# Performance work log

Measured on AMD Instinct MI355X. Metric: run time of the kernel, lower is better.

The kernel has to match this reference:

```python
import jax, jax.numpy as jnp
import numpy as np

N = 20000      # nodes
E = 320000     # edges (avg degree 16)
F_IN = 14
F_OUT = 9
H = 128        # hidden
L = 6          # message passing layers
ED = 3         # edge_dim
MSG_IN = 2 * H + ED  # 259


def _w(k, shape):
    return jax.random.normal(k, shape, jnp.float32) / np.sqrt(shape[0]).astype(np.float32)


def setup_inputs() -> dict:
    key = jax.random.key(0)
    ks = jax.random.split(key, 16)
    x = jax.random.normal(ks[0], (N, F_IN), jnp.float32)
    edge_index = jax.random.randint(ks[1], (2, E), 0, N, jnp.int64)
    edge_attr = jax.random.normal(ks[2], (E, ED), jnp.float32)
    # encoder: Linear(14,128) -> SiLU -> Linear(128,128)
    enc_w1 = _w(ks[3], (F_IN, H)); enc_b1 = jnp.zeros((H,), jnp.float32)
    enc_w2 = _w(ks[4], (H, H));    enc_b2 = jnp.zeros((H,), jnp.float32)
    # L EdgeConv layers: MLP(259->128) -> SiLU -> (128->128), stacked on leading dim
    kc = jax.random.split(ks[5], 2 * L)
    conv_w1 = jnp.stack([_w(kc[i], (MSG_IN, H)) for i in range(L)])
    conv_b1 = jnp.zeros((L, H), jnp.float32)
    conv_w2 = jnp.stack([_w(kc[L + i], (H, H)) for i in range(L)])
    conv_b2 = jnp.zeros((L, H), jnp.float32)
    # decoder: 128->128 SiLU 128->64 SiLU 64->9
    dec_w1 = _w(ks[6], (H, H));       dec_b1 = jnp.zeros((H,), jnp.float32)
    dec_w2 = _w(ks[7], (H, H // 2));  dec_b2 = jnp.zeros((H // 2,), jnp.float32)
    dec_w3 = _w(ks[8], (H // 2, F_OUT)); dec_b3 = jnp.zeros((F_OUT,), jnp.float32)
    return dict(x=x, edge_index=edge_index, edge_attr=edge_attr,
                enc_w1=enc_w1, enc_b1=enc_b1, enc_w2=enc_w2, enc_b2=enc_b2,
                conv_w1=conv_w1, conv_b1=conv_b1, conv_w2=conv_w2, conv_b2=conv_b2,
                dec_w1=dec_w1, dec_b1=dec_b1, dec_w2=dec_w2, dec_b2=dec_b2,
                dec_w3=dec_w3, dec_b3=dec_b3)


def _mlp2(x, w1, b1, w2, b2):
    return jnp.dot(jax.nn.silu(jnp.dot(x, w1) + b1), w2) + b2


def reference(x, edge_index, edge_attr,
              enc_w1, enc_b1, enc_w2, enc_b2,
              conv_w1, conv_b1, conv_w2, conv_b2,
              dec_w1, dec_b1, dec_w2, dec_b2, dec_w3, dec_b3):
    src, dst = edge_index[0], edge_index[1]
    # in-degree for mean aggregation (computed once; structure is fixed)
    deg = jnp.maximum(
        jax.ops.segment_sum(jnp.ones((E,), jnp.float32), dst, num_segments=N), 1.0)
    h = _mlp2(x, enc_w1, enc_b1, enc_w2, enc_b2)  # (N, H)
    for l in range(L):
        # gather-compute-scatter EdgeConv: msg MLP on [h_dst, h_src, edge_attr]
        m_in = jnp.concatenate([h[dst], h[src], edge_attr], axis=-1)  # (E, 2H+ED)
        m = _mlp2(m_in, conv_w1[l], conv_b1[l], conv_w2[l], conv_b2[l])  # (E, H)
        agg = jax.ops.segment_sum(m, dst, num_segments=N) / deg[:, None]  # (N, H)
        h = h + agg  # residual; dropout is identity in eval mode
    h = jax.nn.silu(jnp.dot(h, dec_w1) + dec_b1)
    h = jax.nn.silu(jnp.dot(h, dec_w2) + dec_b2)
    return jnp.dot(h, dec_w3) + dec_b3  # (N, F_OUT)
```

## Files before the change

### kernel.cpp

```cpp
#include <hip/hip_runtime.h>
#include <hip/hip_bf16.h>

#define NN 20000
#define EE 320000
#define HD 128

typedef _Float16 half8 __attribute__((ext_vector_type(8)));
typedef _Float16 half4 __attribute__((ext_vector_type(4)));
typedef _Float16 half2v __attribute__((ext_vector_type(2)));
typedef float floatx4 __attribute__((ext_vector_type(4)));
typedef float float2v __attribute__((ext_vector_type(2)));

__device__ __forceinline__ float silu_f(float x){
  float e = __expf(-x);
  return x * __builtin_amdgcn_rcpf(1.f + e);
}

__device__ __forceinline__ bool ei_is64(const int* __restrict__ ei){
  return (ei[1] | ei[3] | ei[5] | ei[7]) == 0;
}
__device__ __forceinline__ int ei_src(const int* __restrict__ ei, int e, bool is64){
  return is64 ? ei[2*(size_t)e] : ei[e];
}
__device__ __forceinline__ int ei_dst(const int* __restrict__ ei, int e, bool is64){
  return is64 ? ei[2*(size_t)EE + 2*(size_t)e] : ei[EE + e];
}

__global__ __launch_bounds__(256) void sentinel_kernel(float* __restrict__ out, int n, float val){
  int i = blockIdx.x*256 + threadIdx.x;
  if (i < n) out[i] = val;
}

__global__ __launch_bounds__(256) void pack_all_kernel(const float* __restrict__ cw1,
                                                       const float* __restrict__ cw2,
                                                       const float* __restrict__ dw1,
                                                       const float* __restrict__ dw2,
                                                       _Float16* __restrict__ w1p,
                                                       _Float16* __restrict__ w2p,
                                                       _Float16* __restrict__ w1dp,
                                                       _Float16* __restrict__ w2dp,
                                                       int* __restrict__ cur){
  int idx = blockIdx.x*256 + threadIdx.x;
  if (idx >= 319488){
    int j = idx - 319488;
    if (j < NN) cur[j] = 0;
    return;
  }
  if (idx < 196608){
    int j   = idx & 7;
    int ln  = (idx >> 3) & 63;
    int rest= idx >> 9;
    int cb  = rest & 15;
    int rest2 = rest >> 4;
    int ks  = rest2 & 3;
    int l   = rest2 >> 2;
    int k = ks*32 + (ln>>4)*8 + j;
    int c = cb*16 + (ln&15);
    float v = (c < 128) ? cw1[(size_t)l*33152 + (size_t)k*128 + c]
                        : cw1[(size_t)l*33152 + (size_t)(128+k)*128 + (c-128)];
    w1p[idx] = (_Float16)v;
  } else if (idx < 294912){
    int t = idx - 196608;
    int j   = t & 7;
    int ln  = (t >> 3) & 63;
    int rest= t >> 9;
    int cb  = rest & 7;
    int rest2 = rest >> 3;
    int ks  = rest2 & 3;
    int l   = rest2 >> 2;
    int k = ks*32 + (ln>>4)*8 + j;
    int c = cb*16 + (ln&15);
    w2p[t] = (_Float16)cw2[(size_t)l*16384 + (size_t)k*128 + c];
  } else {
    int t2 = idx - 294912;
    if (t2 < 16384){
      int j = t2 & 7, ln = (t2>>3)&63, cb = (t2>>9)&7, ks = t2>>12;
      int k = ks*32 + (ln>>4)*8 + j;
      int c = cb*16 + (ln&15);
      w1dp[t2] = (_Float16)dw1[(size_t)k*128 + c];
    } else {
      int t = t2 - 16384;
      int j = t & 7, ln = (t>>3)&63, cb = (t>>9)&3, ks = t>>11;
      int k = ks*32 + (ln>>4)*8 + j;
      int c = cb*16 + (ln&15);
      w2dp[t] = (_Float16)dw2[(size_t)k*64 + c];
    }
  }
}

__global__ __launch_bounds__(256) void count_kernel(const int* __restrict__ ei,
                                                    int* __restrict__ cnt,
                                                    int* __restrict__ rank){
  int e = blockIdx.x*256 + threadIdx.x;
  bool is64 = ei_is64(ei);
  rank[e] = atomicAdd(&cnt[ei_dst(ei, e, is64)], 1);
}

__global__ __launch_bounds__(1024) void scan_kernel(const int* __restrict__ cntcur,
                                                    int* __restrict__ row_start,
                                                    float* __restrict__ invd){
  __shared__ int part[1024];
  const int t = threadIdx.x;
  const int base = t*20;
  int loc[20];
  int sum = 0;
  #pragma unroll
  for (int i=0;i<20;++i){
    int n = base+i;
    int v = (n < NN) ? cntcur[n] : 0;
    loc[i] = sum; sum += v;
  }
  part[t] = sum;
  __syncthreads();
  for (int off=1; off<1024; off<<=1){
    int v = (t >= off) ? part[t-off] : 0;
    __syncthreads();
    part[t] += v;
    __syncthreads();
  }
  int pre = (t > 0) ? part[t-1] : 0;
  #pragma unroll
  for (int i=0;i<20;++i){
    int n = base+i;
    if (n < NN){
      int rs = pre + loc[i];
      int deg = ((i<19)?loc[i+1]:sum) - loc[i];
      row_start[n] = rs;
      invd[n] = (deg > 0) ? 1.f/(float)deg : 0.f;
    }
  }
  if (t == 1023) row_start[NN] = part[1023];
}

__global__ __launch_bounds__(128) void scatter_encoder_kernel(
    const int* __restrict__ ei, const float* __restrict__ eattr,
    const int* __restrict__ rstart, const int* __restrict__ rank,
    int4* __restrict__ rec,
    const float* __restrict__ x, const float* __restrict__ w1, const float* __restrict__ b1,
    const float* __restrict__ w2, const float* __restrict__ b2,
    float* __restrict__ h, _Float16* __restrict__ hh)
{
  __shared__ float xs[16][14];
  __shared__ float s1[16][128];
  const int tid = threadIdx.x;

  if (blockIdx.x < 2500){
    int e = blockIdx.x*128 + tid;
    bool is64 = ei_is64(ei);
    int s = ei_src(ei, e, is64);
    int d = ei_dst(ei, e, is64);
    int pos = rstart[d] + rank[e];
    int4 r;
    r.x = __float_as_int(eattr[(size_t)e*3+0]);
    r.y = __float_as_int(eattr[(size_t)e*3+1]);
    r.z = __float_as_int(eattr[(size_t)e*3+2]);
    r.w = s*256;
    rec[pos] = r;
    return;
  }

  const int n0 = (blockIdx.x - 2500)*16;
  for (int idx=tid; idx<224; idx+=128){
    int i = idx/14, k = idx%14;
    xs[i][k] = x[(size_t)(n0+i)*14 + k];
  }
  __syncthreads();
  const int o = tid;
  float acc[16];
  float bv = b1[o];
  #pragma unroll
  for (int i=0;i<16;++i) acc[i] = bv;
  for (int k=0;k<14;++k){
    float w = w1[k*128+o];
    #pragma unroll
    for (int i=0;i<16;++i) acc[i] += xs[i][k]*w;
  }
  #pragma unroll
  for (int i=0;i<16;++i) s1[i][o] = silu_f(acc[i]);
  __syncthreads();
  float bv2 = b2[o];
  #pragma unroll
  for (int i=0;i<16;++i) acc[i] = bv2;
  for (int k=0;k<128;k+=4){
    float w0=w2[(k+0)*128+o], w1v=w2[(k+1)*128+o], w2v=w2[(k+2)*128+o], w3v=w2[(k+3)*128+o];
    #pragma unroll
    for (int i=0;i<16;++i){
      float4 sv = *(const float4*)&s1[i][k];
      acc[i] += sv.x*w0 + sv.y*w1v + sv.z*w2v + sv.w*w3v;
    }
  }
  #pragma unroll
  for (int i=0;i<16;++i){
    size_t off = (size_t)(n0+i)*HD + o;
    h[off] = acc[i];
    hh[off] = (_Float16)acc[i];
  }
}

__global__ __launch_bounds__(256) void proj_kernel(
    const _Float16* __restrict__ hh, const _Float16* __restrict__ w1p,
    const float* __restrict__ b1, _Float16* __restrict__ UV)
{
  const int tid = threadIdx.x;
  const int wv  = tid >> 6;
  const int ln  = tid & 63;
  const int q   = ln >> 4;
  const int m   = ln & 15;
  const int n0  = blockIdx.x*16;

  floatx4 acc[4];
  #pragma unroll
  for (int j=0;j<4;++j) acc[j] = (floatx4){0.f,0.f,0.f,0.f};

  #pragma unroll
  for (int ks=0; ks<4; ++ks){
    half8 a = *(const half8*)(hh + (size_t)(n0+m)*HD + ks*32 + q*8);
    const _Float16* wb = w1p + (size_t)(ks*16*64 + ln)*8;
    #pragma unroll
    for (int j=0; j<4; ++j){
      half8 b = *(const half8*)(wb + (size_t)(wv*4+j)*512);
      acc[j] = __builtin_amdgcn_mfma_f32_16x16x32_f16(a, b, acc[j], 0,0,0);
    }
  }
  #pragma unroll
  for (int j=0; j<4; ++j){
    const int c = (wv*4+j)*16 + m;
    const float bias = (c < 128) ? b1[c] : 0.f;
    #pragma unroll
    for (int r=0;r<4;++r)
      UV[(size_t)(n0+q*4+r)*256 + c] = (_Float16)(acc[j][r] + bias);
  }
}

__device__ __forceinline__ float2v edge_contrib(int4 r, half2v v, float2v u,
                                                float2v wc0, float2v wc1, float2v wc2){
  float2v p = u;
  p += __int_as_float(r.x) * wc0;
  p += __int_as_float(r.y) * wc1;
  p += __int_as_float(r.z) * wc2;
  p[0] += (float)v[0];
  p[1] += (float)v[1];
  float2v s;
  s[0] = silu_f(p[0]);
  s[1] = silu_f(p[1]);
  return s;
}

__global__ __launch_bounds__(1024, 8) void layer_kernel(
    const _Float16* __restrict__ UVc, _Float16* __restrict__ UVn,
    const int* __restrict__ row_start, const int4* __restrict__ rec,
    const float* __restrict__ w1e, const float* __restrict__ invd,
    const _Float16* __restrict__ w2p, const float* __restrict__ b2,
    float* __restrict__ h,
    const _Float16* __restrict__ w1pn, const float* __restrict__ b1n,
    int do_proj,
    const _Float16* __restrict__ w1dp, const float* __restrict__ db1,
    const _Float16* __restrict__ w2dp, const float* __restrict__ db2,
    const float* __restrict__ dw3, const float* __restrict__ db3,
    float* __restrict__ out, int do_dec)
{
  __shared__ _Float16 Sl[16][136];
  __shared__ _Float16 hl[16][136];
  __shared__ __align__(16) char ubuf[8576];
  float    (*dl)[132]  = (float(*)[132])ubuf;
  _Float16 (*d1)[136]  = (_Float16(*)[136])ubuf;
  float    (*s2m)[66]  = (float(*)[66])(ubuf + 4352);

  const int tid = threadIdx.x;
  const int w   = __builtin_amdgcn_readfirstlane(tid >> 6);
  const int ln  = tid & 63;
  const int q   = ln >> 4;
  const int m   = ln & 15;
  const int n0  = blockIdx.x*16;

  {
    const int n  = n0 + w;
    const int c0 = ln*2;
    const float2v wc0 = *(const float2v*)(w1e +   0 + c0);
    const float2v wc1 = *(const float2v*)(w1e + 128 + c0);
    const float2v wc2 = *(const float2v*)(w1e + 256 + c0);

    half2v uvp = *(const half2v*)(UVc + (size_t)n*256 + c0);
    float2v u; u[0] = (float)uvp[0]; u[1] = (float)uvp[1];

    const int rs = row_start[n], re = row_start[n+1];
    float2v a0 = {0.f,0.f}, a1 = {0.f,0.f}, a2 = {0.f,0.f}, a3 = {0.f,0.f};

    const int nq = (re - rs) >> 2;
    int e = rs;
    for (int qq = 0; qq < nq; ++qq, e += 4){
      const int4 r0 = rec[e+0];
      const int4 r1 = rec[e+1];
      const int4 r2 = rec[e+2];
      const int4 r3 = rec[e+3];
      const half2v v0 = *(const half2v*)(UVc + (size_t)r0.w + 128 + c0);
      const half2v v1 = *(const half2v*)(UVc + (size_t)r1.w + 128 + c0);
      const half2v v2 = *(const half2v*)(UVc + (size_t)r2.w + 128 + c0);
      const half2v v3 = *(const half2v*)(UVc + (size_t)r3.w + 128 + c0);
      a0 += edge_contrib(r0, v0, u, wc0, wc1, wc2);
      a1 += edge_contrib(r1, v1, u, wc0, wc1, wc2);
      a2 += edge_contrib(r2, v2, u, wc0, wc1, wc2);
      a3 += edge_contrib(r3, v3, u, wc0, wc1, wc2);
    }
    if (e < re){
      const int e1 = (e+1 < re) ? e+1 : e;
      const int e2 = (e+2 < re) ? e+2 : e;
      const int4 r0 = rec[e];
      const int4 r1 = rec[e1];
      const int4 r2 = rec[e2];
      const half2v v0 = *(const half2v*)(UVc + (size_t)r0.w + 128 + c0);
      const half2v v1 = *(const half2v*)(UVc + (size_t)r1.w + 128 + c0);
      const half2v v2 = *(const half2v*)(UVc + (size_t)r2.w + 128 + c0);
      a0 += edge_contrib(r0, v0, u, wc0, wc1, wc2);
      if (e+1 < re) a1 += edge_contrib(r1, v1, u, wc0, wc1, wc2);
      if (e+2 < re) a2 += edge_contrib(r2, v2, u, wc0, wc1, wc2);
    }
    float2v a = (a0 + a1) + (a2 + a3);
    const float iv = invd[n];
    half2v outv; outv[0] = (_Float16)(a[0]*iv); outv[1] = (_Float16)(a[1]*iv);
    *(half2v*)&Sl[w][c0] = outv;
  }
  __syncthreads();

  if (w < 8){
    floatx4 acc = (floatx4){0.f,0.f,0.f,0.f};
    #pragma unroll
    for (int ks=0; ks<4; ++ks){
      half8 a = *(const half8*)&Sl[m][ks*32 + q*8];
      half8 b = *(const half8*)(w2p + (size_t)(ks*8*64 + ln)*8 + (size_t)w*512);
      acc = __builtin_amdgcn_mfma_f32_16x16x32_f16(a, b, acc, 0,0,0);
    }
    const int c = w*16 + m;
    #pragma unroll
    for (int r=0;r<4;++r) dl[q*4+r][c] = acc[r];
  }
  __syncthreads();

  {
    const int row = w;
    const int col = ln*2;
    const float g = (invd[n0 + row] > 0.f) ? 1.f : 0.f;
    float2 hv = *(const float2*)&h[(size_t)(n0+row)*HD + col];
    float2 bv = *(const float2*)&b2[col];
    float2 dv = *(const float2*)&dl[row][col];
    hv.x += dv.x + g*bv.x;
    hv.y += dv.y + g*bv.y;
    if (!do_dec)
      *(float2*)&h[(size_t)(n0+row)*HD + col] = hv;
    half2v p; p[0] = (_Float16)hv.x; p[1] = (_Float16)hv.y;
    *(half2v*)&hl[row][col] = p;
  }
  __syncthreads();

  if (do_proj){
    floatx4 acc = (floatx4){0.f,0.f,0.f,0.f};
    #pragma unroll
    for (int ks=0; ks<4; ++ks){
      half8 a = *(const half8*)&hl[m][ks*32 + q*8];
      half8 b = *(const half8*)(w1pn + (size_t)(ks*16*64 + ln)*8 + (size_t)w*512);
      acc = __builtin_amdgcn_mfma_f32_16x16x32_f16(a, b, acc, 0,0,0);
    }
    const int c = w*16 + m;
    const float bias = (c < 128) ? b1n[c] : 0.f;
    #pragma unroll
    for (int r=0;r<4;++r)
      UVn[(size_t)(n0+q*4+r)*256 + c] = (_Float16)(acc[r] + bias);
  }

  if (do_dec){
    if (w < 8){
      floatx4 acc = (floatx4){0.f,0.f,0.f,0.f};
      #pragma unroll
      for (int ks=0; ks<4; ++ks){
        half8 a = *(const half8*)&hl[m][ks*32 + q*8];
        half8 b = *(const half8*)(w1dp + (size_t)(ks*8*64 + ln)*8 + (size_t)w*512);
        acc = __builtin_amdgcn_mfma_f32_16x16x32_f16(a, b, acc, 0,0,0);
      }
      const int c = w*16 + m;
      const float bv = db1[c];
      #pragma unroll
      for (int r=0;r<4;++r)
        d1[q*4+r][c] = (_Float16)silu_f(acc[r] + bv);
    }
    __syncthreads();

    if (w < 4){
      floatx4 acc = (floatx4){0.f,0.f,0.f,0.f};
      #pragma unroll
      for (int ks=0; ks<4; ++ks){
        half8 a = *(const half8*)&d1[m][ks*32 + q*8];
        half8 b = *(const half8*)(w2dp + (size_t)(ks*4*64 + ln)*8 + (size_t)w*512);
        acc = __builtin_amdgcn_mfma_f32_16x16x32_f16(a, b, acc, 0,0,0);
      }
      const int c = w*16 + m;
      const float bv = db2[c];
      #pragma unroll
      for (int r=0;r<4;++r)
        s2m[q*4+r][c] = silu_f(acc[r] + bv);
    }
    __syncthreads();

    if (tid < 144){
      int i = tid/9, oo = tid%9;
      float a = db3[oo];
      #pragma unroll 8
      for (int k=0;k<64;++k) a += s2m[i][k]*dw3[k*9+oo];
      out[(size_t)(n0+i)*9 + oo] = a;
    }
  }
}

constexpr size_t OFF_H    = 0;
constexpr size_t OFF_HH   = 10240000;
constexpr size_t OFF_UVA  = 15360000;
constexpr size_t OFF_UVB  = 25600000;
constexpr size_t OFF_INVD = 35840000;
constexpr size_t OFF_RS   = 35920000;
constexpr size_t OFF_CUR  = 36000064;
constexpr size_t OFF_REC  = 36080064;
constexpr size_t OFF_RANK = 41200064;
constexpr size_t OFF_W1P  = 42480064;
constexpr size_t OFF_W2P  = 42873280;
constexpr size_t OFF_DW1P = 43069888;
constexpr size_t OFF_DW2P = 43102656;
constexpr size_t WS_NEEDED= 43119040;

extern "C" void kernel_launch(void* const* d_in, const int* in_sizes, int n_in,
                              void* d_out, int out_size, void* d_ws, size_t ws_size,
                              hipStream_t stream)
{
  float* out = (float*)d_out;
  const int nout_blk = (out_size + 255)/256;

  static const int EXP_SIZES[17] = {280000,640000,960000,1792,128,16384,128,
                                    198912,768,98304,768,16384,128,8192,64,576,9};
  if (n_in != 17){
    sentinel_kernel<<<nout_blk, 256, 0, stream>>>(out, out_size, 2.0e7f + (float)n_in*1.0e3f);
    return;
  }
  for (int i = 0; i < 17; ++i){
    if (in_sizes[i] != EXP_SIZES[i]){
      int sz = in_sizes[i] < 99999 ? in_sizes[i] : 99999;
      sentinel_kernel<<<nout_blk, 256, 0, stream>>>(out, out_size,
          1.0e7f + (float)i*1.0e5f + (float)sz);
      return;
    }
  }
  if (ws_size < WS_NEEDED){
    sentinel_kernel<<<nout_blk, 256, 0, stream>>>(out, out_size, 1.0e6f);
    return;
  }

  const float* x       = (const float*)d_in[0];
  const int*   ei      = (const int*)  d_in[1];
  const float* eattr   = (const float*)d_in[2];
  const float* enc_w1  = (const float*)d_in[3];
  const float* enc_b1  = (const float*)d_in[4];
  const float* enc_w2  = (const float*)d_in[5];
  const float* enc_b2  = (const float*)d_in[6];
  const float* conv_w1 = (const float*)d_in[7];
  const float* conv_b1 = (const float*)d_in[8];
  const float* conv_w2 = (const float*)d_in[9];
  const float* conv_b2 = (const float*)d_in[10];
  const float* dec_w1  = (const float*)d_in[11];
  const float* dec_b1  = (const float*)d_in[12];
  const float* dec_w2  = (const float*)d_in[13];
  const float* dec_b2  = (const float*)d_in[14];
  const float* dec_w3  = (const float*)d_in[15];
  const float* dec_b3  = (const float*)d_in[16];

  char* ws = (char*)d_ws;
  float*    h     = (float*)   (ws + OFF_H);
  _Float16* hh    = (_Float16*)(ws + OFF_HH);
  _Float16* UVa   = (_Float16*)(ws + OFF_UVA);
  _Float16* UVb   = (_Float16*)(ws + OFF_UVB);
  float*    invd  = (float*)   (ws + OFF_INVD);
  int*      rstart= (int*)     (ws + OFF_RS);
  int*      cur   = (int*)     (ws + OFF_CUR);
  int4*     rec   = (int4*)    (ws + OFF_REC);
  int*      rank  = (int*)     (ws + OFF_RANK);
  _Float16* w1p   = (_Float16*)(ws + OFF_W1P);
  _Float16* w2p   = (_Float16*)(ws + OFF_W2P);
  _Float16* w1dp  = (_Float16*)(ws + OFF_DW1P);
  _Float16* w2dp  = (_Float16*)(ws + OFF_DW2P);

  pack_all_kernel<<<1327, 256, 0, stream>>>(conv_w1, conv_w2, dec_w1, dec_w2,
                                            w1p, w2p, w1dp, w2dp, cur);
  count_kernel<<<EE/256, 256, 0, stream>>>(ei, cur, rank);
  scan_kernel<<<1, 1024, 0, stream>>>(cur, rstart, invd);
  scatter_encoder_kernel<<<3750, 128, 0, stream>>>(ei, eattr, rstart, rank, rec,
                                                   x, enc_w1, enc_b1, enc_w2, enc_b2,
                                                   h, hh);
  proj_kernel<<<NN/16, 256, 0, stream>>>(hh, w1p, conv_b1, UVa);
  for (int l=0; l<6; ++l){
    _Float16* UVc = (l & 1) ? UVb : UVa;
    _Float16* UVn = (l & 1) ? UVa : UVb;
    const int lp = (l < 5) ? l+1 : 0;
    layer_kernel<<<NN/16, 1024, 0, stream>>>(UVc, UVn, rstart, rec,
                                             conv_w1 + (size_t)l*33152 + 32768,
                                             invd,
                                             w2p + (size_t)l*16384,
                                             conv_b2 + (size_t)l*128,
                                             h,
                                             w1p + (size_t)lp*32768,
                                             conv_b1 + (size_t)lp*128,
                                             (l < 5) ? 1 : 0,
                                             w1dp, dec_b1, w2dp, dec_b2,
                                             dec_w3, dec_b3, out,
                                             (l == 5) ? 1 : 0);
  }
}
```

Before: 331.1 us.

## Sort nodes by descending degree to balance warps within layer blocks

The scan kernel now builds a counting-sort permutation of nodes by descending in-degree, and each layer block processes 16 permuted nodes instead of 16 consecutive ones. Grouping nodes of similar degree into a block reduces the time waves sit idle waiting for the highest-degree node before the block-wide barrier, and launching heavy blocks first helps tail balance. In exchange, h, UV and output rows are read and written through an indirection, which scatters memory access and loses contiguous row locality, and the single-block scan does extra serial work.

```diff
diff --git a/kernel.cpp b/kernel.cpp
--- a/kernel.cpp
+++ b/kernel.cpp
@@ -98,16 +98,20 @@
 
 __global__ __launch_bounds__(1024) void scan_kernel(const int* __restrict__ cntcur,
                                                     int* __restrict__ row_start,
-                                                    float* __restrict__ invd){
+                                                    float* __restrict__ invd,
+                                                    int* __restrict__ perm){
   __shared__ int part[1024];
+  __shared__ int hist[256];
   const int t = threadIdx.x;
   const int base = t*20;
   int loc[20];
+  int truedeg[20];
   int sum = 0;
   #pragma unroll
   for (int i=0;i<20;++i){
     int n = base+i;
     int v = (n < NN) ? cntcur[n] : 0;
+    truedeg[i] = v;
     loc[i] = sum; sum += v;
   }
   part[t] = sum;
@@ -123,13 +127,37 @@
   for (int i=0;i<20;++i){
     int n = base+i;
     if (n < NN){
-      int rs = pre + loc[i];
-      int deg = ((i<19)?loc[i+1]:sum) - loc[i];
-      row_start[n] = rs;
-      invd[n] = (deg > 0) ? 1.f/(float)deg : 0.f;
+      row_start[n] = pre + loc[i];
+      invd[n] = (truedeg[i] > 0) ? 1.f/(float)truedeg[i] : 0.f;
     }
   }
   if (t == 1023) row_start[NN] = part[1023];
+
+  if (t < 256) hist[t] = 0;
+  __syncthreads();
+  #pragma unroll
+  for (int i=0;i<20;++i){
+    int n = base+i;
+    if (n < NN){
+      int b = 255 - (truedeg[i] < 255 ? truedeg[i] : 255);
+      atomicAdd(&hist[b], 1);
+    }
+  }
+  __syncthreads();
+  if (t == 0){
+    int s = 0;
+    for (int b=0;b<256;++b){ int v = hist[b]; hist[b] = s; s += v; }
+  }
+  __syncthreads();
+  #pragma unroll
+  for (int i=0;i<20;++i){
+    int n = base+i;
+    if (n < NN){
+      int b = 255 - (truedeg[i] < 255 ? truedeg[i] : 255);
+      int pos = atomicAdd(&hist[b], 1);
+      perm[pos] = n;
+    }
+  }
 }
 
 __global__ __launch_bounds__(128) void scatter_encoder_kernel(
@@ -250,6 +278,7 @@
     const _Float16* __restrict__ UVc, _Float16* __restrict__ UVn,
     const int* __restrict__ row_start, const int4* __restrict__ rec,
     const float* __restrict__ w1e, const float* __restrict__ invd,
+    const int* __restrict__ perm,
     const _Float16* __restrict__ w2p, const float* __restrict__ b2,
     float* __restrict__ h,
     const _Float16* __restrict__ w1pn, const float* __restrict__ b1n,
@@ -261,6 +290,7 @@
 {
   __shared__ _Float16 Sl[16][136];
   __shared__ _Float16 hl[16][136];
+  __shared__ int pnode[16];
   __shared__ __align__(16) char ubuf[8576];
   float    (*dl)[132]  = (float(*)[132])ubuf;
   _Float16 (*d1)[136]  = (_Float16(*)[136])ubuf;
@@ -274,7 +304,8 @@
   const int n0  = blockIdx.x*16;
 
   {
-    const int n  = n0 + w;
+    const int n  = perm[n0 + w];
+    if (ln == 0) pnode[w] = n;
     const int c0 = ln*2;
     const float2v wc0 = *(const float2v*)(w1e +   0 + c0);
     const float2v wc1 = *(const float2v*)(w1e + 128 + c0);
@@ -338,15 +369,16 @@
 
   {
     const int row = w;
+    const int pn  = pnode[row];
     const int col = ln*2;
-    const float g = (invd[n0 + row] > 0.f) ? 1.f : 0.f;
-    float2 hv = *(const float2*)&h[(size_t)(n0+row)*HD + col];
+    const float g = (invd[pn] > 0.f) ? 1.f : 0.f;
+    float2 hv = *(const float2*)&h[(size_t)pn*HD + col];
     float2 bv = *(const float2*)&b2[col];
     float2 dv = *(const float2*)&dl[row][col];
     hv.x += dv.x + g*bv.x;
     hv.y += dv.y + g*bv.y;
     if (!do_dec)
-      *(float2*)&h[(size_t)(n0+row)*HD + col] = hv;
+      *(float2*)&h[(size_t)pn*HD + col] = hv;
     half2v p; p[0] = (_Float16)hv.x; p[1] = (_Float16)hv.y;
     *(half2v*)&hl[row][col] = p;
   }
@@ -364,7 +396,7 @@
     const float bias = (c < 128) ? b1n[c] : 0.f;
     #pragma unroll
     for (int r=0;r<4;++r)
-      UVn[(size_t)(n0+q*4+r)*256 + c] = (_Float16)(acc[r] + bias);
+      UVn[(size_t)pnode[q*4+r]*256 + c] = (_Float16)(acc[r] + bias);
   }
 
   if (do_dec){
@@ -405,7 +437,7 @@
       float a = db3[oo];
       #pragma unroll 8
       for (int k=0;k<64;++k) a += s2m[i][k]*dw3[k*9+oo];
-      out[(size_t)(n0+i)*9 + oo] = a;
+      out[(size_t)pnode[i]*9 + oo] = a;
     }
   }
 }
@@ -419,11 +451,12 @@
 constexpr size_t OFF_CUR  = 36000064;
 constexpr size_t OFF_REC  = 36080064;
 constexpr size_t OFF_RANK = 41200064;
-constexpr size_t OFF_W1P  = 42480064;
-constexpr size_t OFF_W2P  = 42873280;
-constexpr size_t OFF_DW1P = 43069888;
-constexpr size_t OFF_DW2P = 43102656;
-constexpr size_t WS_NEEDED= 43119040;
+constexpr size_t OFF_PERM = 42480064;
+constexpr size_t OFF_W1P  = 42560064;
+constexpr size_t OFF_W2P  = 42953280;
+constexpr size_t OFF_DW1P = 43149888;
+constexpr size_t OFF_DW2P = 43182656;
+constexpr size_t WS_NEEDED= 43199040;
 
 extern "C" void kernel_launch(void* const* d_in, const int* in_sizes, int n_in,
                               void* d_out, int out_size, void* d_ws, size_t ws_size,
@@ -479,6 +512,7 @@
   int*      cur   = (int*)     (ws + OFF_CUR);
   int4*     rec   = (int4*)    (ws + OFF_REC);
   int*      rank  = (int*)     (ws + OFF_RANK);
+  int*      perm  = (int*)     (ws + OFF_PERM);
   _Float16* w1p   = (_Float16*)(ws + OFF_W1P);
   _Float16* w2p   = (_Float16*)(ws + OFF_W2P);
   _Float16* w1dp  = (_Float16*)(ws + OFF_DW1P);
@@ -487,7 +521,7 @@
   pack_all_kernel<<<1327, 256, 0, stream>>>(conv_w1, conv_w2, dec_w1, dec_w2,
                                             w1p, w2p, w1dp, w2dp, cur);
   count_kernel<<<EE/256, 256, 0, stream>>>(ei, cur, rank);
-  scan_kernel<<<1, 1024, 0, stream>>>(cur, rstart, invd);
+  scan_kernel<<<1, 1024, 0, stream>>>(cur, rstart, invd, perm);
   scatter_encoder_kernel<<<3750, 128, 0, stream>>>(ei, eattr, rstart, rank, rec,
                                                    x, enc_w1, enc_b1, enc_w2, enc_b2,
                                                    h, hh);
@@ -498,7 +532,7 @@
     const int lp = (l < 5) ? l+1 : 0;
     layer_kernel<<<NN/16, 1024, 0, stream>>>(UVc, UVn, rstart, rec,
                                              conv_w1 + (size_t)l*33152 + 32768,
-                                             invd,
+                                             invd, perm,
                                              w2p + (size_t)l*16384,
                                              conv_b2 + (size_t)l*128,
                                              h,
```

New measurement: 335.4 us. Within noise of the previous version (+1.3%).
